# Optimization experiments

Measured on AMD Instinct MI355X. Metric: run time of the kernel, lower is better.

The kernel has to match this reference:

```python
import jax, jax.numpy as jnp
import numpy as np

HIDDEN = 1024
NUM_HEADS = 16
HEAD_DIM = 64
B, S = 2, 2048


def setup_inputs() -> dict:
    key = jax.random.key(0)
    k1, k2, k3 = jax.random.split(key, 3)
    x = jax.random.normal(k1, (B, S, HIDDEN), dtype=jnp.float32)
    # xavier-uniform style scaling for the projection weights
    lim_qkv = (6.0 / (HIDDEN + 3 * NUM_HEADS * HEAD_DIM)) ** 0.5
    lim_o = (6.0 / (NUM_HEADS * HEAD_DIM + HIDDEN)) ** 0.5
    w_qkv = jax.random.uniform(k2, (HIDDEN, 3 * NUM_HEADS * HEAD_DIM), jnp.float32, -lim_qkv, lim_qkv)
    w_o = jax.random.uniform(k3, (NUM_HEADS * HEAD_DIM, HIDDEN), jnp.float32, -lim_o, lim_o)
    return {"x": x, "w_qkv": w_qkv, "w_o": w_o}


def reference(x, w_qkv, w_o):
    b, s, _ = x.shape
    qkv = jnp.einsum('bsh,hf->bsf', x, w_qkv)               # [b, s, 3*H*D]
    qkv = qkv.reshape(b, s, 3, NUM_HEADS, HEAD_DIM)
    q = jnp.transpose(qkv[:, :, 0], (0, 2, 1, 3))           # [b, h, s, d]
    k = jnp.transpose(qkv[:, :, 1], (0, 2, 3, 1))           # [b, h, d, s]
    v = jnp.transpose(qkv[:, :, 2], (0, 2, 1, 3))           # [b, h, s, d]
    scores = jnp.einsum('bhqd,bhdk->bhqk', q, k) / jnp.sqrt(jnp.float32(HEAD_DIM))
    scores = jax.nn.softmax(scores, axis=-1)                # [b, h, q, k]
    # NOTE: faithful to source bug: sums over q, output indexed by k
    values = jnp.einsum('bhqk,bhkd->bhkd', scores, v)       # [b, h, s, d]
    values = jnp.transpose(values, (0, 2, 1, 3)).reshape(b, s, NUM_HEADS * HEAD_DIM)
    return jnp.einsum('bsf,fh->bsh', values, w_o)
```

## Files before the change

### kernel.cpp

```cpp
#include <hip/hip_runtime.h>
#include <stdint.h>


#define DEV static __device__ __forceinline__

typedef unsigned short u16;
typedef __attribute__((ext_vector_type(4))) float f32x4;
typedef __attribute__((ext_vector_type(16))) float f32x16;
typedef __bf16 bf16x8 __attribute__((ext_vector_type(8)));
typedef __attribute__((ext_vector_type(8))) unsigned short u16x8;
typedef __attribute__((ext_vector_type(4))) unsigned short u16x4;

#define QSCALE 0.18033688011112042f

DEV u16 f2bf(float f) {
    unsigned u = __builtin_bit_cast(unsigned, f);
    u += 0x7fffu + ((u >> 16) & 1u);
    return (u16)(u >> 16);
}
DEV float bf2f(u16 h) {
    unsigned u = ((unsigned)h) << 16;
    return __builtin_bit_cast(float, u);
}

DEV void async_copy16(const void* g, void* l) {
    __builtin_amdgcn_global_load_lds(
        (__attribute__((address_space(1))) void*)(g),
        (__attribute__((address_space(3))) void*)(l), 16, 0, 0);
}


__global__ __launch_bounds__(256) void cast_f32_bf16(
    const float* __restrict__ src, u16* __restrict__ dst, int n4) {
    int i = blockIdx.x * 256 + threadIdx.x;
    if (i >= n4) return;
    f32x4 v = *(const f32x4*)(src + (size_t)i * 4);
    u16x4 o;
#pragma unroll
    for (int j = 0; j < 4; j++) o[j] = f2bf(v[j]);
    *(u16x4*)(dst + (size_t)i * 4) = o;
}

__global__ __launch_bounds__(256) void transpose_cast(
    const float* __restrict__ src, u16* __restrict__ dst, int rows, int cols) {
    __shared__ float tile[32][33];
    int c0 = blockIdx.x * 32, r0 = blockIdx.y * 32;
    int tx = threadIdx.x, ty = threadIdx.y;
#pragma unroll
    for (int i = 0; i < 4; i++)
        tile[ty + i * 8][tx] = src[(size_t)(r0 + ty + i * 8) * cols + c0 + tx];
    __syncthreads();
#pragma unroll
    for (int i = 0; i < 4; i++)
        dst[(size_t)(c0 + ty + i * 8) * rows + r0 + tx] = f2bf(tile[tx][ty + i * 8]);
}

__global__ __launch_bounds__(256) void gemm_qkv(
    const u16* __restrict__ A, const u16* __restrict__ Bt,
    u16* __restrict__ qb, u16* __restrict__ kb, u16* __restrict__ vb) {
    __shared__ __align__(16) u16 smem[128 * 136];
    u16* As = smem;
    u16* Bs = smem + 4096;
    const int t = threadIdx.x;
    const int wave = t >> 6;
    const int lane = t & 63;
    const int quad = lane >> 4;
    const int l16 = lane & 15;
    const int wr = wave >> 1;
    const int wc = wave & 1;
    const int m0 = blockIdx.y * 128;
    const int n0 = blockIdx.x * 128;

    f32x4 acc[4][4];
#pragma unroll
    for (int i = 0; i < 4; i++)
#pragma unroll
        for (int j = 0; j < 4; j++) acc[i][j] = {0.f, 0.f, 0.f, 0.f};

    for (int kt = 0; kt < 1024; kt += 32) {
#pragma unroll
        for (int i = 0; i < 2; i++) {
            int idx = i * 256 + t;
            int row = idx >> 2, kc = idx & 3;
            async_copy16(A + (size_t)(m0 + row) * 1024 + kt + kc * 8, &As[idx * 8]);
            async_copy16(Bt + (size_t)(n0 + row) * 1024 + kt + kc * 8, &Bs[idx * 8]);
        }
        __syncthreads();
        bf16x8 af[4], bfr[4];
#pragma unroll
        for (int mt = 0; mt < 4; mt++)
            af[mt] = *(const bf16x8*)&As[(wr * 64 + mt * 16 + l16) * 32 + quad * 8];
#pragma unroll
        for (int nt = 0; nt < 4; nt++)
            bfr[nt] = *(const bf16x8*)&Bs[(wc * 64 + nt * 16 + l16) * 32 + quad * 8];
#pragma unroll
        for (int mt = 0; mt < 4; mt++)
#pragma unroll
            for (int nt = 0; nt < 4; nt++)
                acc[mt][nt] = __builtin_amdgcn_mfma_f32_16x16x32_bf16(
                    af[mt], bfr[nt], acc[mt][nt], 0, 0, 0);
        __syncthreads();
    }

    const int tsel = n0 >> 10;
    u16* dst = tsel == 0 ? qb : (tsel == 1 ? kb : vb);
    const float scl = tsel == 0 ? QSCALE : 1.0f;
#pragma unroll
    for (int mt = 0; mt < 4; mt++)
#pragma unroll
        for (int nt = 0; nt < 4; nt++) {
            int nn = wc * 64 + nt * 16 + l16;
#pragma unroll
            for (int r = 0; r < 4; r++) {
                int mm = wr * 64 + mt * 16 + quad * 4 + r;
                smem[mm * 136 + nn] = f2bf(acc[mt][nt][r] * scl);
            }
        }
    __syncthreads();
    const int col0 = (l16) * 8;
    const int rowb = (t >> 4);
    const int h0 = (n0 & 1023) >> 6;
#pragma unroll
    for (int i = 0; i < 8; i++) {
        int row = i * 16 + rowb;
        u16x8 v = *(const u16x8*)&smem[row * 136 + col0];
        int h = h0 + (col0 >> 6), d = col0 & 63;
        int mm = m0 + row;
        int b = mm >> 11, s = mm & 2047;
        *(u16x8*)&dst[((size_t)((b * 16 + h) * 2048 + s)) * 64 + d] = v;
    }
}

__global__ __launch_bounds__(256) void gemm_out(
    const u16* __restrict__ A, const u16* __restrict__ Bt,
    float* __restrict__ out) {
    __shared__ __align__(16) u16 As[64 * 32];
    __shared__ __align__(16) u16 Bs[128 * 32];
    const int m0 = blockIdx.y * 64;
    const int n0 = blockIdx.x * 128;
    const int t = threadIdx.x;
    const int wave = t >> 6, lane = t & 63;
    const int quad = lane >> 4, l16 = lane & 15;
    const int wr = wave >> 1, wc = wave & 1;

    f32x4 acc[2][4];
#pragma unroll
    for (int i = 0; i < 2; i++)
#pragma unroll
        for (int j = 0; j < 4; j++) acc[i][j] = {0.f, 0.f, 0.f, 0.f};

    for (int kt = 0; kt < 1024; kt += 32) {
        async_copy16(A + (size_t)(m0 + (t >> 2)) * 1024 + kt + (t & 3) * 8, &As[t * 8]);
#pragma unroll
        for (int i = 0; i < 2; i++) {
            int idx = i * 256 + t;
            int row = idx >> 2, kc = idx & 3;
            async_copy16(Bt + (size_t)(n0 + row) * 1024 + kt + kc * 8, &Bs[idx * 8]);
        }
        __syncthreads();
        bf16x8 af[2], bfr[4];
#pragma unroll
        for (int mt = 0; mt < 2; mt++)
            af[mt] = *(const bf16x8*)&As[(wr * 32 + mt * 16 + l16) * 32 + quad * 8];
#pragma unroll
        for (int nt = 0; nt < 4; nt++)
            bfr[nt] = *(const bf16x8*)&Bs[(wc * 64 + nt * 16 + l16) * 32 + quad * 8];
#pragma unroll
        for (int mt = 0; mt < 2; mt++)
#pragma unroll
            for (int nt = 0; nt < 4; nt++)
                acc[mt][nt] = __builtin_amdgcn_mfma_f32_16x16x32_bf16(
                    af[mt], bfr[nt], acc[mt][nt], 0, 0, 0);
        __syncthreads();
    }
#pragma unroll
    for (int nt = 0; nt < 4; nt++) {
        int nn = n0 + wc * 64 + nt * 16 + l16;
#pragma unroll
        for (int mt = 0; mt < 2; mt++) {
#pragma unroll
            for (int r = 0; r < 4; r++) {
                int mm = m0 + wr * 32 + mt * 16 + quad * 4 + r;
                out[(size_t)mm * 1024 + nn] = acc[mt][nt][r];
            }
        }
    }
}

__global__ __launch_bounds__(256) void attn_pass1(
    const u16* __restrict__ qb, const u16* __restrict__ kb,
    float* __restrict__ lp) {
    __shared__ __align__(16) u16 Ks0[128 * 32];
    __shared__ __align__(16) u16 Ks1[128 * 32];
    const int t = threadIdx.x;
    const int wave = t >> 6;
    const int lane = t & 63;
    const int l32 = lane & 31, half = lane >> 5;
    const int kchunk = blockIdx.x & 1;
    const int qblk = (blockIdx.x >> 1) & 15;
    const int bh = blockIdx.x >> 5;
    const int q0 = qblk * 128 + wave * 32;

    const u16* Qr = qb + (size_t)(bh * 2048 + q0 + l32) * 64 + half * 8;
    bf16x8 a[4];
#pragma unroll
    for (int f = 0; f < 4; f++) a[f] = *(const bf16x8*)&Qr[f * 16];

    const u16* Kbase = kb + (size_t)(bh * 2048 + kchunk * 1024) * 64;
    const int srow = t >> 2, sc = (t & 3) * 8;

    float lsum[16];
#pragma unroll
    for (int r = 0; r < 16; r++) lsum[r] = 0.f;

    for (int kt = 0; kt < 8; kt++) {
#pragma unroll
        for (int rr = 0; rr < 2; rr++) {
            const u16* src = Kbase + (size_t)(kt * 128 + rr * 64 + srow) * 64 + sc;
            async_copy16(src, &Ks0[rr * 2048 + t * 8]);
            async_copy16(src + 32, &Ks1[rr * 2048 + t * 8]);
        }
        __syncthreads();
#pragma unroll
        for (int sub = 0; sub < 4; sub++) {
            const int row = sub * 32 + l32;
            bf16x8 bfr[4];
            bfr[0] = *(const bf16x8*)&Ks0[row * 32 + half * 8];
            bfr[1] = *(const bf16x8*)&Ks0[row * 32 + 16 + half * 8];
            bfr[2] = *(const bf16x8*)&Ks1[row * 32 + half * 8];
            bfr[3] = *(const bf16x8*)&Ks1[row * 32 + 16 + half * 8];
            f32x16 acc;
#pragma unroll
            for (int r = 0; r < 16; r++) acc[r] = 0.f;
#pragma unroll
            for (int f = 0; f < 4; f++)
                acc = __builtin_amdgcn_mfma_f32_32x32x16_bf16(a[f], bfr[f], acc, 0, 0, 0);
#pragma unroll
            for (int r = 0; r < 16; r++)
                lsum[r] += __builtin_amdgcn_exp2f(acc[r]);
        }
        __syncthreads();
    }
#pragma unroll
    for (int r = 0; r < 16; r++) {
        float v = lsum[r];
        v += __shfl_xor(v, 1);
        v += __shfl_xor(v, 2);
        v += __shfl_xor(v, 4);
        v += __shfl_xor(v, 8);
        v += __shfl_xor(v, 16);
        lsum[r] = v;
    }
    if (l32 == 0) {
        float* dst = lp + kchunk * 65536 + bh * 2048 + q0 + half * 4;
#pragma unroll
        for (int r = 0; r < 16; r++)
            dst[(r & 3) + 8 * (r >> 2)] = lsum[r];
    }
}

__global__ __launch_bounds__(256) void attn_pass2(
    const u16* __restrict__ qb, const u16* __restrict__ kb,
    const float* __restrict__ lp, float* __restrict__ cp) {
    __shared__ __align__(16) u16 Qs0[128 * 32];
    __shared__ __align__(16) u16 Qs1[128 * 32];
    __shared__ __align__(16) float li_lds[1024];
    const int t = threadIdx.x;
    const int wave = t >> 6;
    const int lane = t & 63;
    const int l32 = lane & 31, half = lane >> 5;
    const int qchunk = blockIdx.x & 1;
    const int kblk = (blockIdx.x >> 1) & 15;
    const int bh = blockIdx.x >> 5;
    const int k0 = kblk * 128 + wave * 32;

    {
        const int base = bh * 2048 + qchunk * 1024;
        f32x4 p0 = *(const f32x4*)&lp[base + t * 4];
        f32x4 p1 = *(const f32x4*)&lp[65536 + base + t * 4];
        f32x4 li;
#pragma unroll
        for (int j = 0; j < 4; j++) li[j] = 1.0f / (p0[j] + p1[j]);
        *(f32x4*)&li_lds[t * 4] = li;
    }

    const u16* Kr = kb + (size_t)(bh * 2048 + k0 + l32) * 64 + half * 8;
    bf16x8 b[4];
#pragma unroll
    for (int f = 0; f < 4; f++) b[f] = *(const bf16x8*)&Kr[f * 16];

    const u16* Qbase = qb + (size_t)(bh * 2048 + qchunk * 1024) * 64;
    const int srow = t >> 2, sc = (t & 3) * 8;

    float cs = 0.f;
    __syncthreads();

    for (int qt = 0; qt < 8; qt++) {
#pragma unroll
        for (int rr = 0; rr < 2; rr++) {
            const u16* src = Qbase + (size_t)(qt * 128 + rr * 64 + srow) * 64 + sc;
            async_copy16(src, &Qs0[rr * 2048 + t * 8]);
            async_copy16(src + 32, &Qs1[rr * 2048 + t * 8]);
        }
        __syncthreads();
#pragma unroll
        for (int sub = 0; sub < 4; sub++) {
            const int row = sub * 32 + l32;
            bf16x8 af[4];
            af[0] = *(const bf16x8*)&Qs0[row * 32 + half * 8];
            af[1] = *(const bf16x8*)&Qs0[row * 32 + 16 + half * 8];
            af[2] = *(const bf16x8*)&Qs1[row * 32 + half * 8];
            af[3] = *(const bf16x8*)&Qs1[row * 32 + 16 + half * 8];
            f32x16 acc;
#pragma unroll
            for (int r = 0; r < 16; r++) acc[r] = 0.f;
#pragma unroll
            for (int f = 0; f < 4; f++)
                acc = __builtin_amdgcn_mfma_f32_32x32x16_bf16(af[f], b[f], acc, 0, 0, 0);
            const float* lr = &li_lds[qt * 128 + sub * 32 + half * 4];
            f32x4 li0 = *(const f32x4*)&lr[0];
            f32x4 li1 = *(const f32x4*)&lr[8];
            f32x4 li2 = *(const f32x4*)&lr[16];
            f32x4 li3 = *(const f32x4*)&lr[24];
#pragma unroll
            for (int r = 0; r < 4; r++) cs += __builtin_amdgcn_exp2f(acc[r]) * li0[r];
#pragma unroll
            for (int r = 0; r < 4; r++) cs += __builtin_amdgcn_exp2f(acc[4 + r]) * li1[r];
#pragma unroll
            for (int r = 0; r < 4; r++) cs += __builtin_amdgcn_exp2f(acc[8 + r]) * li2[r];
#pragma unroll
            for (int r = 0; r < 4; r++) cs += __builtin_amdgcn_exp2f(acc[12 + r]) * li3[r];
        }
        __syncthreads();
    }
    cs += __shfl_xor(cs, 32);
    if (lane < 32)
        cp[qchunk * 65536 + bh * 2048 + k0 + lane] = cs;
}

__global__ __launch_bounds__(256) void scale_v(
    const u16* __restrict__ vb, const float* __restrict__ cp,
    u16* __restrict__ valsb) {
    int tid = blockIdx.x * 256 + threadIdx.x;
    int base = tid << 3;
    int bh = base >> 17;
    int rem = base & 131071;
    int s = rem >> 6;
    int d0 = rem & 63;
    int ci = bh * 2048 + s;
    float cs = cp[ci] + cp[65536 + ci];
    u16x8 v = *(const u16x8*)(vb + (size_t)base);
    u16x8 o;
#pragma unroll
    for (int i = 0; i < 8; i++) o[i] = f2bf(bf2f(v[i]) * cs);
    int b = bh >> 4, h = bh & 15;
    *(u16x8*)(valsb + (size_t)((b * 2048 + s) * 1024) + h * 64 + d0) = o;
}


extern "C" void kernel_launch(void* const* d_in, const int* in_sizes, int n_in,
                              void* d_out, int out_size, void* d_ws, size_t ws_size,
                              hipStream_t stream) {
    const float* x    = (const float*)d_in[0];
    const float* wqkv = (const float*)d_in[1];
    const float* wo   = (const float*)d_in[2];
    float* out = (float*)d_out;
    char* ws = (char*)d_ws;

    u16* xb      = (u16*)(ws);
    u16* wqkvT   = (u16*)(ws + 8388608);
    u16* woT     = (u16*)(ws + 14680064);
    u16* qb      = (u16*)(ws + 16777216);
    u16* kb      = (u16*)(ws + 25165824);
    u16* vb      = (u16*)(ws + 33554432);
    u16* valsb   = (u16*)(ws + 42467328);
    float* lp    = (float*)(ws);
    float* cp    = (float*)(ws + 1048576);

    cast_f32_bf16<<<4096, 256, 0, stream>>>(x, xb, 1048576);
    transpose_cast<<<dim3(96, 32), dim3(32, 8), 0, stream>>>(wqkv, wqkvT, 1024, 3072);
    transpose_cast<<<dim3(32, 32), dim3(32, 8), 0, stream>>>(wo, woT, 1024, 1024);
    gemm_qkv<<<dim3(24, 32), 256, 0, stream>>>(xb, wqkvT, qb, kb, vb);
    attn_pass1<<<1024, 256, 0, stream>>>(qb, kb, lp);
    attn_pass2<<<1024, 256, 0, stream>>>(qb, kb, lp, cp);
    scale_v<<<2048, 256, 0, stream>>>(vb, cp, valsb);
    gemm_out<<<dim3(8, 64), 256, 0, stream>>>(valsb, woT, out);
}
```

Baseline: 200.9 us.

## Load K/Q fragments directly from global memory in attention passes, drop LDS staging

Both attention passes stop staging K (pass1) and Q (pass2) tiles through shared memory with async copies and block barriers. Each wave now loads its MFMA operand fragments straight from global memory (relying on L2/L1 since all four waves read the same rows), with a partially unrolled loop. MFMA blocks are bracketed by s_setprio to favour matrix issue. This removes LDS traffic and __syncthreads stalls, but each wave issues its own global loads, so there is redundant traffic and memory latency is exposed without explicit double-buffering.

```diff
diff --git a/kernel.cpp b/kernel.cpp
--- a/kernel.cpp
+++ b/kernel.cpp
@@ -187,11 +187,10 @@
     }
 }
 
+
 __global__ __launch_bounds__(256) void attn_pass1(
     const u16* __restrict__ qb, const u16* __restrict__ kb,
     float* __restrict__ lp) {
-    __shared__ __align__(16) u16 Ks0[128 * 32];
-    __shared__ __align__(16) u16 Ks1[128 * 32];
     const int t = threadIdx.x;
     const int wave = t >> 6;
     const int lane = t & 63;
@@ -206,40 +205,29 @@
 #pragma unroll
     for (int f = 0; f < 4; f++) a[f] = *(const bf16x8*)&Qr[f * 16];
 
-    const u16* Kbase = kb + (size_t)(bh * 2048 + kchunk * 1024) * 64;
-    const int srow = t >> 2, sc = (t & 3) * 8;
+    const u16* Kp = kb + (size_t)(bh * 2048 + kchunk * 1024 + l32) * 64 + half * 8;
 
     float lsum[16];
 #pragma unroll
     for (int r = 0; r < 16; r++) lsum[r] = 0.f;
 
-    for (int kt = 0; kt < 8; kt++) {
-#pragma unroll
-        for (int rr = 0; rr < 2; rr++) {
-            const u16* src = Kbase + (size_t)(kt * 128 + rr * 64 + srow) * 64 + sc;
-            async_copy16(src, &Ks0[rr * 2048 + t * 8]);
-            async_copy16(src + 32, &Ks1[rr * 2048 + t * 8]);
-        }
-        __syncthreads();
-#pragma unroll
-        for (int sub = 0; sub < 4; sub++) {
-            const int row = sub * 32 + l32;
-            bf16x8 bfr[4];
-            bfr[0] = *(const bf16x8*)&Ks0[row * 32 + half * 8];
-            bfr[1] = *(const bf16x8*)&Ks0[row * 32 + 16 + half * 8];
-            bfr[2] = *(const bf16x8*)&Ks1[row * 32 + half * 8];
-            bfr[3] = *(const bf16x8*)&Ks1[row * 32 + 16 + half * 8];
-            f32x16 acc;
-#pragma unroll
-            for (int r = 0; r < 16; r++) acc[r] = 0.f;
-#pragma unroll
-            for (int f = 0; f < 4; f++)
-                acc = __builtin_amdgcn_mfma_f32_32x32x16_bf16(a[f], bfr[f], acc, 0, 0, 0);
-#pragma unroll
-            for (int r = 0; r < 16; r++)
-                lsum[r] += __builtin_amdgcn_exp2f(acc[r]);
-        }
-        __syncthreads();
+#pragma unroll 2
+    for (int sub = 0; sub < 32; sub++) {
+        const u16* Kr = Kp + (size_t)sub * 2048;
+        bf16x8 bfr[4];
+#pragma unroll
+        for (int f = 0; f < 4; f++) bfr[f] = *(const bf16x8*)&Kr[f * 16];
+        f32x16 acc;
+#pragma unroll
+        for (int r = 0; r < 16; r++) acc[r] = 0.f;
+        __builtin_amdgcn_s_setprio(1);
+#pragma unroll
+        for (int f = 0; f < 4; f++)
+            acc = __builtin_amdgcn_mfma_f32_32x32x16_bf16(a[f], bfr[f], acc, 0, 0, 0);
+        __builtin_amdgcn_s_setprio(0);
+#pragma unroll
+        for (int r = 0; r < 16; r++)
+            lsum[r] += __builtin_amdgcn_exp2f(acc[r]);
     }
 #pragma unroll
     for (int r = 0; r < 16; r++) {
@@ -262,8 +250,6 @@
 __global__ __launch_bounds__(256) void attn_pass2(
     const u16* __restrict__ qb, const u16* __restrict__ kb,
     const float* __restrict__ lp, float* __restrict__ cp) {
-    __shared__ __align__(16) u16 Qs0[128 * 32];
-    __shared__ __align__(16) u16 Qs1[128 * 32];
     __shared__ __align__(16) float li_lds[1024];
     const int t = threadIdx.x;
     const int wave = t >> 6;
@@ -289,49 +275,38 @@
 #pragma unroll
     for (int f = 0; f < 4; f++) b[f] = *(const bf16x8*)&Kr[f * 16];
 
-    const u16* Qbase = qb + (size_t)(bh * 2048 + qchunk * 1024) * 64;
-    const int srow = t >> 2, sc = (t & 3) * 8;
+    const u16* Qp = qb + (size_t)(bh * 2048 + qchunk * 1024 + l32) * 64 + half * 8;
 
     float cs = 0.f;
     __syncthreads();
 
-    for (int qt = 0; qt < 8; qt++) {
-#pragma unroll
-        for (int rr = 0; rr < 2; rr++) {
-            const u16* src = Qbase + (size_t)(qt * 128 + rr * 64 + srow) * 64 + sc;
-            async_copy16(src, &Qs0[rr * 2048 + t * 8]);
-            async_copy16(src + 32, &Qs1[rr * 2048 + t * 8]);
-        }
-        __syncthreads();
-#pragma unroll
-        for (int sub = 0; sub < 4; sub++) {
-            const int row = sub * 32 + l32;
-            bf16x8 af[4];
-            af[0] = *(const bf16x8*)&Qs0[row * 32 + half * 8];
-            af[1] = *(const bf16x8*)&Qs0[row * 32 + 16 + half * 8];
-            af[2] = *(const bf16x8*)&Qs1[row * 32 + half * 8];
-            af[3] = *(const bf16x8*)&Qs1[row * 32 + 16 + half * 8];
-            f32x16 acc;
-#pragma unroll
-            for (int r = 0; r < 16; r++) acc[r] = 0.f;
-#pragma unroll
-            for (int f = 0; f < 4; f++)
-                acc = __builtin_amdgcn_mfma_f32_32x32x16_bf16(af[f], b[f], acc, 0, 0, 0);
-            const float* lr = &li_lds[qt * 128 + sub * 32 + half * 4];
-            f32x4 li0 = *(const f32x4*)&lr[0];
-            f32x4 li1 = *(const f32x4*)&lr[8];
-            f32x4 li2 = *(const f32x4*)&lr[16];
-            f32x4 li3 = *(const f32x4*)&lr[24];
-#pragma unroll
-            for (int r = 0; r < 4; r++) cs += __builtin_amdgcn_exp2f(acc[r]) * li0[r];
-#pragma unroll
-            for (int r = 0; r < 4; r++) cs += __builtin_amdgcn_exp2f(acc[4 + r]) * li1[r];
-#pragma unroll
-            for (int r = 0; r < 4; r++) cs += __builtin_amdgcn_exp2f(acc[8 + r]) * li2[r];
-#pragma unroll
-            for (int r = 0; r < 4; r++) cs += __builtin_amdgcn_exp2f(acc[12 + r]) * li3[r];
-        }
-        __syncthreads();
+#pragma unroll 2
+    for (int sub = 0; sub < 32; sub++) {
+        const u16* Qr2 = Qp + (size_t)sub * 2048;
+        bf16x8 af[4];
+#pragma unroll
+        for (int f = 0; f < 4; f++) af[f] = *(const bf16x8*)&Qr2[f * 16];
+        f32x16 acc;
+#pragma unroll
+        for (int r = 0; r < 16; r++) acc[r] = 0.f;
+        __builtin_amdgcn_s_setprio(1);
+#pragma unroll
+        for (int f = 0; f < 4; f++)
+            acc = __builtin_amdgcn_mfma_f32_32x32x16_bf16(af[f], b[f], acc, 0, 0, 0);
+        __builtin_amdgcn_s_setprio(0);
+        const float* lr = &li_lds[sub * 32 + half * 4];
+        f32x4 li0 = *(const f32x4*)&lr[0];
+        f32x4 li1 = *(const f32x4*)&lr[8];
+        f32x4 li2 = *(const f32x4*)&lr[16];
+        f32x4 li3 = *(const f32x4*)&lr[24];
+#pragma unroll
+        for (int r = 0; r < 4; r++) cs += __builtin_amdgcn_exp2f(acc[r]) * li0[r];
+#pragma unroll
+        for (int r = 0; r < 4; r++) cs += __builtin_amdgcn_exp2f(acc[4 + r]) * li1[r];
+#pragma unroll
+        for (int r = 0; r < 4; r++) cs += __builtin_amdgcn_exp2f(acc[8 + r]) * li2[r];
+#pragma unroll
+        for (int r = 0; r < 4; r++) cs += __builtin_amdgcn_exp2f(acc[12 + r]) * li3[r];
     }
     cs += __shfl_xor(cs, 32);
     if (lane < 32)
@@ -354,7 +329,7 @@
 #pragma unroll
     for (int i = 0; i < 8; i++) o[i] = f2bf(bf2f(v[i]) * cs);
     int b = bh >> 4, h = bh & 15;
-    *(u16x8*)(valsb + (size_t)((b * 2048 + s) * 1024) + h * 64 + d0) = o;
+    *(u16x8*)&valsb[(size_t)((b * 2048 + s) * 1024) + h * 64 + d0] = o;
 }
 
 
```

After: 261.3 us. 1.3x slower.
